# Performance work log

Hardware: AMD Instinct MI355X
Metric: run time of the kernel (lower is better)

Reference implementation:

```python
import jax, jax.numpy as jnp
import numpy as np

B, L, D = 16, 196, 512
M = 4096            # existing memory slots
DIS_MEM_LEN = 4096  # M+1 > DIS_MEM_LEN -> eviction always triggers (static shapes)


def setup_inputs() -> dict:
    key = jax.random.key(0)
    ks = jax.random.split(key, 10)
    x = jax.random.normal(ks[0], (B, L, D), jnp.float32)
    feat_mem = jax.random.normal(ks[1], (B, M, D), jnp.float32)
    # freq >= 6 so rm_mask = (freq > 5) is guaranteed nonempty (matches torch
    # branch `if rm_mask.sum() > 0`) and asserts freq != 0, min <= freq hold.
    freq_mem = 6 + jax.random.randint(ks[2], (B, M), 0, 50, jnp.int32)
    min_mem = jax.random.randint(ks[3], (B, M), 0, 6, jnp.int32)
    s = float(1.0 / np.sqrt(D))
    Wv = jax.random.uniform(ks[4], (D, D), jnp.float32, -s, s)
    bv = jax.random.uniform(ks[5], (D,), jnp.float32, -s, s)
    Wu = jax.random.uniform(ks[6], (D, D), jnp.float32, -s, s)
    bu = jax.random.uniform(ks[7], (D,), jnp.float32, -s, s)
    Ww = jax.random.uniform(ks[8], (D, 1), jnp.float32, -s, s)
    bw = jax.random.uniform(ks[9], (1,), jnp.float32, -s, s)
    return dict(x=x, feat_mem=feat_mem, freq_mem=freq_mem, min_mem=min_mem,
                Wv=Wv, bv=bv, Wu=Wu, bu=bu, Ww=Ww, bw=bw)


def reference(x, feat_mem, freq_mem, min_mem, Wv, bv, Wu, bu, Ww, bw):
    bs = x.shape[0]
    cls = x[:, :1, :]                                  # [B, 1, D]
    feat = jnp.concatenate([feat_mem, cls], axis=1)    # [B, M+1, D]
    zero = jnp.zeros((bs, 1), jnp.int32)
    freq = jnp.concatenate([freq_mem, zero], axis=1)   # [B, M+1]
    mn = jnp.concatenate([min_mem, zero], axis=1)      # [B, M+1]

    # gated attention score: sigmoid(Linear(tanh(Lv x) * sigmoid(Lu x)))
    attn_v = jnp.tanh(feat @ Wv + bv)
    attn_u = jax.nn.sigmoid(feat @ Wu + bu)
    attn_score = jax.nn.sigmoid((attn_v * attn_u) @ Ww + bw)  # [B, M+1, 1]

    # eval-mode cur_iter_mask = ones; feat is detached in z in the original
    z = jnp.sum(attn_score * jax.lax.stop_gradient(feat), axis=1)  # [B, D]

    # update_freq_mem: mask is all ones -> +1 everywhere
    freq = freq + 1
    # update_min_mem: argmin of attn_score along memory dim, scatter +1
    attn_idx = jnp.argmin(attn_score[..., 0], axis=1)  # [B]
    mn = mn.at[jnp.arange(bs), attn_idx].add(1)

    # eviction: M+1 > dis_mem_len, remove argmax(min/freq * (freq>5)) per batch
    rm_mask = freq > 5
    ratio = mn.astype(jnp.float32) / freq.astype(jnp.float32) * rm_mask
    rm_idx = jnp.argmax(ratio, axis=1)                 # [B]
    col = jnp.arange(freq.shape[1])[None, :]
    is_rm = col == rm_idx[:, None]                     # [B, M+1] one True per row
    # stable argsort puts kept indices first (in original order), removed one last
    order = jnp.argsort(is_rm, axis=1, stable=True)[:, : freq.shape[1] - 1]
    feat_out = jnp.take_along_axis(feat, order[..., None], axis=1)  # [B, M, D]
    freq_out = jnp.take_along_axis(freq, order, axis=1)             # [B, M]
    min_out = jnp.take_along_axis(mn, order, axis=1)                # [B, M]
    return z, feat_out, freq_out, min_out
```

## Files before the change

kernel.cpp:

```cpp
#include <hip/hip_runtime.h>
#include <cmath>

#define NB 16
#define MM 4096
#define MP1 4097
#define DD 512
#define LSEQ 196
#define NRB 65
#define MARGIN 0.05f
#define CANDMAX 128

typedef float f32x4 __attribute__((ext_vector_type(4)));
typedef short bf16x8 __attribute__((ext_vector_type(8)));
typedef unsigned short u16x8 __attribute__((ext_vector_type(8)));

static __device__ __forceinline__ unsigned short bf16_rne(float x) {
  union { float f; unsigned u; } c; c.f = x;
  unsigned u = c.u;
  u += 0x7fffu + ((u >> 16) & 1u);
  return (unsigned short)(u >> 16);
}
static __device__ __forceinline__ float bf16_to_f(unsigned short h) {
  union { unsigned u; float f; } c; c.u = ((unsigned)h) << 16;
  return c.f;
}
static __device__ __forceinline__ unsigned cvt_pk_bf16(float lo, float hi) {
  unsigned r;
  asm("v_cvt_pk_bf16_f32 %0, %1, %2" : "=v"(r) : "v"(lo), "v"(hi));
  return r;
}
static __device__ __forceinline__ float sig_prec(float v) { return 1.0f / (1.0f + expf(-v)); }
static __device__ __forceinline__ float sig_fast(float v) { return 1.0f / (1.0f + __expf(-v)); }
static __device__ __forceinline__ float tanh_fast(float v) { return fmaf(2.0f, sig_fast(2.0f * v), -1.0f); }

__global__ __launch_bounds__(256) void k_packW(const float* __restrict__ Wv,
                                               const float* __restrict__ Wu,
                                               unsigned short* __restrict__ Bc) {
  const int gid = blockIdx.x * 256 + threadIdx.x;
  const int l = gid & 63;
  const int ksg = (gid >> 6) & 15;
  const int ctg = (gid >> 10) & 31;
  const int mat = gid >> 15;
  const float* W = mat ? Wu : Wv;
  const int col = ctg * 16 + (l & 15);
  const int kb = ksg * 32 + (l >> 4) * 8;
  u16x8 hi;
#pragma unroll
  for (int i = 0; i < 8; ++i) hi[i] = bf16_rne(W[(size_t)(kb + i) * DD + col]);
  const int ctg2 = ctg * 2 + mat;
  *(u16x8*)(Bc + ((size_t)(ctg2 * 16 + ksg)) * 512 + l * 8) = hi;
}

__global__ __launch_bounds__(1024) void k_scores(
    const float* __restrict__ x, const float* __restrict__ feat_mem,
    const unsigned short* __restrict__ Bc,
    const float* __restrict__ bv, const float* __restrict__ bu,
    const float* __restrict__ Ww, const float* __restrict__ bw,
    float* __restrict__ logits, float* __restrict__ zacc) {
  const int rb = blockIdx.x, b = blockIdx.y;
  const int row0 = rb * 64;
  const int tid = threadIdx.x, wave = tid >> 6, l = tid & 63;

  __shared__ __align__(16) unsigned short A[4 * 8192];
  __shared__ float sred[16][64];
  __shared__ float sscore[64];

  {
    const int r = tid >> 4;
    const int j = tid & 15;
    const int grow = row0 + r;
    const float* srcrow = nullptr;
    if (grow < MM) srcrow = feat_mem + ((size_t)b * MM + grow) * DD;
    else if (grow == MM) srcrow = x + (size_t)b * LSEQ * DD;
    const int rt = r >> 4, lrow = r & 15;
#pragma unroll
    for (int it = 0; it < 8; ++it) {
      const int k0 = it * 64 + j * 4;
      const float4 v = srcrow ? *(const float4*)(srcrow + k0) : make_float4(0.f, 0.f, 0.f, 0.f);
      const int kc = k0 >> 7, kin = k0 & 127;
      const int ks = kin >> 5, lhi = (kin >> 3) & 3, ii = kin & 7;
      uint2 p;
      p.x = cvt_pk_bf16(v.x, v.y);
      p.y = cvt_pk_bf16(v.z, v.w);
      *(uint2*)(A + kc * 8192 + (ks * 4 + rt) * 512 + (lhi * 16 + lrow) * 8 + ii) = p;
    }
  }
  __syncthreads();

  f32x4 acc[4][4];
#pragma unroll
  for (int i = 0; i < 4; ++i)
#pragma unroll
    for (int j2 = 0; j2 < 4; ++j2) acc[i][j2] = (f32x4){0.f, 0.f, 0.f, 0.f};

  const unsigned short* Bwave = Bc + ((size_t)(wave * 4) * 16) * 512 + l * 8;
#pragma unroll 4
  for (int ksg = 0; ksg < 16; ++ksg) {
    const unsigned short* Ab = A + (ksg >> 2) * 8192 + ((ksg & 3) * 4) * 512 + l * 8;
    bf16x8 hiA[4];
#pragma unroll
    for (int rt = 0; rt < 4; ++rt) hiA[rt] = *(const bf16x8*)(Ab + rt * 512);
#pragma unroll
    for (int ct = 0; ct < 4; ++ct) {
      const bf16x8 bb = *(const bf16x8*)(Bwave + (size_t)(ct * 16 + ksg) * 512);
#pragma unroll
      for (int rt = 0; rt < 4; ++rt)
        acc[rt][ct] = __builtin_amdgcn_mfma_f32_16x16x32_bf16(hiA[rt], bb, acc[rt][ct], 0, 0, 0);
    }
  }

  float prow[4][4];
#pragma unroll
  for (int i = 0; i < 4; ++i)
#pragma unroll
    for (int j2 = 0; j2 < 4; ++j2) prow[i][j2] = 0.f;
#pragma unroll
  for (int gp = 0; gp < 2; ++gp) {
    const int col = (wave * 2 + gp) * 16 + (l & 15);
    const float bvc = bv[col], buc = bu[col], wwc = Ww[col];
#pragma unroll
    for (int rt = 0; rt < 4; ++rt)
#pragma unroll
      for (int rr = 0; rr < 4; ++rr) {
        const float vv = tanh_fast(acc[rt][2 * gp][rr] + bvc);
        const float uu = sig_fast(acc[rt][2 * gp + 1][rr] + buc);
        prow[rt][rr] = fmaf(vv * uu, wwc, prow[rt][rr]);
      }
  }
#pragma unroll
  for (int off = 1; off < 16; off <<= 1)
#pragma unroll
    for (int rt = 0; rt < 4; ++rt)
#pragma unroll
      for (int rr = 0; rr < 4; ++rr) prow[rt][rr] += __shfl_xor(prow[rt][rr], off, 64);

  if ((l & 15) == 0) {
#pragma unroll
    for (int rt = 0; rt < 4; ++rt)
#pragma unroll
      for (int rr = 0; rr < 4; ++rr) sred[wave][rt * 16 + (l >> 4) * 4 + rr] = prow[rt][rr];
  }
  __syncthreads();

  if (tid < 64) {
    float s = 0.f;
#pragma unroll
    for (int w = 0; w < 16; ++w) s += sred[w][tid];
    const int row = row0 + tid;
    if (row < MP1) logits[(size_t)b * MP1 + row] = s;
    sscore[tid] = sig_fast(s + bw[0]);
  }
  __syncthreads();

  {
    const int d = tid & 511;
    const int rh = tid >> 9;
    const int kc = d >> 7, kin = d & 127;
    const int ks = kin >> 5, lhi = (kin >> 3) & 3, ii = kin & 7;
    const unsigned short* Abase = A + kc * 8192 + ks * 4 * 512 + lhi * 16 * 8 + ii;
    float zp = 0.f;
#pragma unroll
    for (int rr2 = 0; rr2 < 32; ++rr2) {
      const int r2 = rh * 32 + rr2;
      const float a = bf16_to_f(Abase[(r2 >> 4) * 512 + (r2 & 15) * 8]);
      zp = fmaf(sscore[r2], a, zp);
    }
    atomicAdd(&zacc[(size_t)b * DD + d], zp);
  }
}

__global__ __launch_bounds__(256) void k_cand(const float* __restrict__ logits,
                                              int* __restrict__ cand,
                                              int* __restrict__ cnt) {
  const int b = blockIdx.x, tid = threadIdx.x;
  __shared__ float sv[256];
  __shared__ int scnt;
  float m = INFINITY;
  for (int i = tid; i < MP1; i += 256) m = fminf(m, logits[(size_t)b * MP1 + i]);
  sv[tid] = m;
  __syncthreads();
  for (int s = 128; s >= 1; s >>= 1) {
    if (tid < s) sv[tid] = fminf(sv[tid], sv[tid + s]);
    __syncthreads();
  }
  const float minv = sv[0];
  if (tid == 0) scnt = 0;
  __syncthreads();
  for (int i = tid; i < MP1; i += 256) {
    if (logits[(size_t)b * MP1 + i] <= minv + MARGIN) {
      const int p = atomicAdd(&scnt, 1);
      if (p < CANDMAX) cand[b * CANDMAX + p] = i;
    }
  }
  __syncthreads();
  if (tid == 0) cnt[b] = (scnt < CANDMAX) ? scnt : CANDMAX;
}

__global__ __launch_bounds__(256) void k_refine(
    const float* __restrict__ x, const float* __restrict__ feat_mem,
    const float* __restrict__ Wv, const float* __restrict__ bv,
    const float* __restrict__ Wu, const float* __restrict__ bu,
    const float* __restrict__ Ww,
    const int* __restrict__ cand, const int* __restrict__ cnt,
    float* __restrict__ candpart) {
  const int b = blockIdx.z, c = blockIdx.y, cb = blockIdx.x;
  if (c >= cnt[b]) return;
  const int row = cand[b * CANDMAX + c];
  const int tid = threadIdx.x;
  const int jl = tid & 63;
  const int ks = tid >> 6;
  const int col = cb * 64 + jl;
  __shared__ __align__(16) float sfeat[DD];
  __shared__ float sredv[4][64];
  __shared__ float sredu[4][64];
  const float* src = (row < MM) ? feat_mem + ((size_t)b * MM + row) * DD
                                : x + (size_t)b * LSEQ * DD;
  if (tid < 128) ((float4*)sfeat)[tid] = ((const float4*)src)[tid];
  __syncthreads();
  float v = 0.f, u = 0.f;
  const float* wvp = Wv + (size_t)(ks * 128) * DD + col;
  const float* wup = Wu + (size_t)(ks * 128) * DD + col;
#pragma unroll 8
  for (int k = 0; k < 128; ++k) {
    const float a = sfeat[ks * 128 + k];
    v = fmaf(a, wvp[(size_t)k * DD], v);
    u = fmaf(a, wup[(size_t)k * DD], u);
  }
  sredv[ks][jl] = v;
  sredu[ks][jl] = u;
  __syncthreads();
  if (tid < 64) {
    const float vv = (sredv[0][jl] + sredv[1][jl]) + (sredv[2][jl] + sredv[3][jl]);
    const float uu = (sredu[0][jl] + sredu[1][jl]) + (sredu[2][jl] + sredu[3][jl]);
    float g = tanhf(vv + bv[col]) * sig_prec(uu + bu[col]) * Ww[col];
#pragma unroll
    for (int off = 1; off < 64; off <<= 1) g += __shfl_xor(g, off, 64);
    if (jl == 0) candpart[((size_t)b * CANDMAX + c) * 8 + cb] = g;
  }
}

__global__ __launch_bounds__(256) void k_finalize2(
    const int* __restrict__ cand, const float* __restrict__ candpart,
    const int* __restrict__ cnt, const int* __restrict__ freq_mem,
    const int* __restrict__ min_mem, const float* __restrict__ zacc,
    float* __restrict__ out_z, float* __restrict__ out_freq,
    float* __restrict__ out_min, int* __restrict__ rm_attn) {
  const int b = blockIdx.x, tid = threadIdx.x;
  __shared__ float sv[256];
  __shared__ int si[256];
  __shared__ int sn[256], sd[256], sj[256];
  __shared__ int s_attn, s_rm;

  const int n = cnt[b];
  float v = INFINITY;
  int idx = MP1;
  if (tid < n) {
    const float* p = candpart + ((size_t)b * CANDMAX + tid) * 8;
    v = ((p[0] + p[1]) + (p[2] + p[3])) + ((p[4] + p[5]) + (p[6] + p[7]));
    idx = cand[b * CANDMAX + tid];
  }
  sv[tid] = v; si[tid] = idx;
  __syncthreads();
  for (int s = 128; s >= 1; s >>= 1) {
    if (tid < s) {
      const float v2 = sv[tid + s]; const int i2 = si[tid + s];
      if (v2 < sv[tid] || (v2 == sv[tid] && i2 < si[tid])) { sv[tid] = v2; si[tid] = i2; }
    }
    __syncthreads();
  }
  if (tid == 0) s_attn = si[0];
  __syncthreads();
  const int attn = s_attn;

  int bn = -1, bd = 1, bj = 0;
  for (int i = tid; i < MP1; i += 256) {
    int num, den;
    if (i < MM) {
      den = freq_mem[(size_t)b * MM + i] + 1;
      num = min_mem[(size_t)b * MM + i] + (i == attn ? 1 : 0);
      if (den <= 5) num = 0;
    } else { den = 1; num = 0; }
    if (num * bd > bn * den) { bn = num; bd = den; bj = i; }
  }
  sn[tid] = bn; sd[tid] = bd; sj[tid] = bj;
  __syncthreads();
  for (int s = 128; s >= 1; s >>= 1) {
    if (tid < s) {
      const int n2 = sn[tid + s], d2 = sd[tid + s], j2 = sj[tid + s];
      const int lft = n2 * sd[tid], rgt = sn[tid] * d2;
      if (lft > rgt || (lft == rgt && j2 < sj[tid])) { sn[tid] = n2; sd[tid] = d2; sj[tid] = j2; }
    }
    __syncthreads();
  }
  if (tid == 0) { s_rm = sj[0]; rm_attn[b * 2] = attn; rm_attn[b * 2 + 1] = sj[0]; }
  __syncthreads();
  const int rm = s_rm;

  for (int i = tid; i < MM; i += 256) {
    const int src = (i < rm) ? i : i + 1;
    int fv, mv;
    if (src < MM) {
      fv = freq_mem[(size_t)b * MM + src] + 1;
      mv = min_mem[(size_t)b * MM + src] + (src == attn ? 1 : 0);
    } else {
      fv = 1; mv = (attn == MM) ? 1 : 0;
    }
    out_freq[(size_t)b * MM + i] = (float)fv;
    out_min[(size_t)b * MM + i] = (float)mv;
  }
  for (int d = tid; d < DD; d += 256) out_z[(size_t)b * DD + d] = zacc[(size_t)b * DD + d];
}

__global__ __launch_bounds__(256) void k_gather(
    const float* __restrict__ feat_mem, const float* __restrict__ x,
    const int* __restrict__ rm_attn, float* __restrict__ out_feat) {
  const int b = blockIdx.y;
  const int rm = rm_attn[b * 2 + 1];
  const int row = blockIdx.x * 4 + (threadIdx.x >> 6);
  const int lane = threadIdx.x & 63;
  const int src = (row < rm) ? row : row + 1;
  const float* sp = (src < MM) ? (feat_mem + ((size_t)b * MM + src) * DD)
                               : (x + (size_t)b * LSEQ * DD);
  float* dp = out_feat + ((size_t)b * MM + row) * DD;
  const float4 v0 = reinterpret_cast<const float4*>(sp)[lane];
  const float4 v1 = reinterpret_cast<const float4*>(sp)[lane + 64];
  reinterpret_cast<float4*>(dp)[lane] = v0;
  reinterpret_cast<float4*>(dp)[lane + 64] = v1;
}

extern "C" void kernel_launch(void* const* d_in, const int* in_sizes, int n_in,
                              void* d_out, int out_size, void* d_ws, size_t ws_size,
                              hipStream_t stream) {
  const float* x        = (const float*)d_in[0];
  const float* feat_mem = (const float*)d_in[1];
  const int*   freq_mem = (const int*)d_in[2];
  const int*   min_mem  = (const int*)d_in[3];
  const float* Wv       = (const float*)d_in[4];
  const float* bv       = (const float*)d_in[5];
  const float* Wu       = (const float*)d_in[6];
  const float* bu       = (const float*)d_in[7];
  const float* Ww       = (const float*)d_in[8];
  const float* bw       = (const float*)d_in[9];

  float* ws       = (float*)d_ws;
  float* logits   = ws;
  float* zacc     = ws + NB * MP1;
  float* candpart = zacc + NB * DD;
  int*   cand     = (int*)(candpart + NB * CANDMAX * 8);
  int*   cnt      = cand + NB * CANDMAX;
  int*   rm_attn  = cnt + NB;
  unsigned short* Bc = (unsigned short*)(rm_attn + 32);

  float* out_z    = (float*)d_out;
  float* out_feat = out_z + NB * DD;
  float* out_freq = out_feat + (size_t)NB * MM * DD;
  float* out_min  = out_freq + (size_t)NB * MM;

  hipMemsetAsync(zacc, 0, NB * DD * sizeof(float), stream);
  hipMemsetAsync(cnt, 0, NB * sizeof(int), stream);

  k_packW<<<dim3(256), dim3(256), 0, stream>>>(Wv, Wu, Bc);
  k_scores<<<dim3(NRB, NB), dim3(1024), 0, stream>>>(x, feat_mem, Bc, bv, bu, Ww, bw,
                                                     logits, zacc);
  k_cand<<<dim3(NB), dim3(256), 0, stream>>>(logits, cand, cnt);
  k_refine<<<dim3(8, CANDMAX, NB), dim3(256), 0, stream>>>(x, feat_mem, Wv, bv, Wu, bu, Ww,
                                                           cand, cnt, candpart);
  k_finalize2<<<dim3(NB), dim3(256), 0, stream>>>(cand, candpart, cnt, freq_mem, min_mem, zacc,
                                                  out_z, out_freq, out_min, rm_attn);
  k_gather<<<dim3(MM / 4, NB), dim3(256), 0, stream>>>(feat_mem, x, rm_attn, out_feat);
}
```

Measured before the change: 224.1 us.

## Swizzle LDS A-tile layout, double-buffer B fragment loads, batch global loads

```diff
diff --git a/kernel.cpp b/kernel.cpp
--- a/kernel.cpp
+++ b/kernel.cpp
@@ -73,16 +73,22 @@
     if (grow < MM) srcrow = feat_mem + ((size_t)b * MM + grow) * DD;
     else if (grow == MM) srcrow = x + (size_t)b * LSEQ * DD;
     const int rt = r >> 4, lrow = r & 15;
+    float4 v[8];
+#pragma unroll
+    for (int it = 0; it < 8; ++it)
+      v[it] = srcrow ? *(const float4*)(srcrow + it * 64 + j * 4)
+                     : make_float4(0.f, 0.f, 0.f, 0.f);
 #pragma unroll
     for (int it = 0; it < 8; ++it) {
       const int k0 = it * 64 + j * 4;
-      const float4 v = srcrow ? *(const float4*)(srcrow + k0) : make_float4(0.f, 0.f, 0.f, 0.f);
       const int kc = k0 >> 7, kin = k0 & 127;
       const int ks = kin >> 5, lhi = (kin >> 3) & 3, ii = kin & 7;
       uint2 p;
-      p.x = cvt_pk_bf16(v.x, v.y);
-      p.y = cvt_pk_bf16(v.z, v.w);
-      *(uint2*)(A + kc * 8192 + (ks * 4 + rt) * 512 + (lhi * 16 + lrow) * 8 + ii) = p;
+      p.x = cvt_pk_bf16(v[it].x, v[it].y);
+      p.y = cvt_pk_bf16(v[it].z, v[it].w);
+      const int U = kc * 8192 + (ks * 4 + rt) * 512 + lhi * 128 +
+                    ((lrow * 8) ^ (lhi << 3) ^ ((ks & 1) << 5)) + ii;
+      *(uint2*)(A + U) = p;
     }
   }
   __syncthreads();
@@ -94,20 +100,41 @@
     for (int j2 = 0; j2 < 4; ++j2) acc[i][j2] = (f32x4){0.f, 0.f, 0.f, 0.f};
 
   const unsigned short* Bwave = Bc + ((size_t)(wave * 4) * 16) * 512 + l * 8;
-#pragma unroll 4
-  for (int ksg = 0; ksg < 16; ++ksg) {
-    const unsigned short* Ab = A + (ksg >> 2) * 8192 + ((ksg & 3) * 4) * 512 + l * 8;
-    bf16x8 hiA[4];
-#pragma unroll
-    for (int rt = 0; rt < 4; ++rt) hiA[rt] = *(const bf16x8*)(Ab + rt * 512);
-#pragma unroll
-    for (int ct = 0; ct < 4; ++ct) {
-      const bf16x8 bb = *(const bf16x8*)(Bwave + (size_t)(ct * 16 + ksg) * 512);
-#pragma unroll
-      for (int rt = 0; rt < 4; ++rt)
-        acc[rt][ct] = __builtin_amdgcn_mfma_f32_16x16x32_bf16(hiA[rt], bb, acc[rt][ct], 0, 0, 0);
-    }
-  }
+  const int lanebase = l * 8 ^ ((l >> 4) << 3);
+  bf16x8 bbA[4], bbB[4];
+
+#define BLOAD(dst, ksg)                                                     \
+  {                                                                         \
+    _Pragma("unroll")                                                       \
+    for (int ct = 0; ct < 4; ++ct)                                          \
+      dst[ct] = *(const bf16x8*)(Bwave + (size_t)(ct * 16 + (ksg)) * 512);  \
+  }
+#define KSTEP(CUR, NXT, ksg, last)                                                        \
+  {                                                                                       \
+    if (!(last)) BLOAD(NXT, (ksg) + 1);                                                   \
+    const unsigned short* Ab =                                                            \
+        A + ((ksg) >> 2) * 8192 + ((ksg) & 3) * 2048 + (lanebase ^ (((ksg) & 1) << 5));   \
+    const bf16x8 hiA0 = *(const bf16x8*)(Ab);                                             \
+    const bf16x8 hiA1 = *(const bf16x8*)(Ab + 512);                                       \
+    const bf16x8 hiA2 = *(const bf16x8*)(Ab + 1024);                                      \
+    const bf16x8 hiA3 = *(const bf16x8*)(Ab + 1536);                                      \
+    _Pragma("unroll")                                                                     \
+    for (int ct = 0; ct < 4; ++ct) {                                                      \
+      acc[0][ct] = __builtin_amdgcn_mfma_f32_16x16x32_bf16(hiA0, CUR[ct], acc[0][ct], 0, 0, 0); \
+      acc[1][ct] = __builtin_amdgcn_mfma_f32_16x16x32_bf16(hiA1, CUR[ct], acc[1][ct], 0, 0, 0); \
+      acc[2][ct] = __builtin_amdgcn_mfma_f32_16x16x32_bf16(hiA2, CUR[ct], acc[2][ct], 0, 0, 0); \
+      acc[3][ct] = __builtin_amdgcn_mfma_f32_16x16x32_bf16(hiA3, CUR[ct], acc[3][ct], 0, 0, 0); \
+    }                                                                                     \
+  }
+
+  BLOAD(bbA, 0);
+#pragma unroll
+  for (int kk = 0; kk < 8; ++kk) {
+    KSTEP(bbA, bbB, 2 * kk, false);
+    KSTEP(bbB, bbA, 2 * kk + 1, (kk == 7));
+  }
+#undef BLOAD
+#undef KSTEP
 
   float prow[4][4];
 #pragma unroll
@@ -157,13 +184,14 @@
     const int rh = tid >> 9;
     const int kc = d >> 7, kin = d & 127;
     const int ks = kin >> 5, lhi = (kin >> 3) & 3, ii = kin & 7;
-    const unsigned short* Abase = A + kc * 8192 + ks * 4 * 512 + lhi * 16 * 8 + ii;
+    const int ubase = kc * 8192 + ks * 2048 + lhi * 128 + ii;
+    const int swz = (lhi << 3) ^ ((ks & 1) << 5);
     float zp = 0.f;
 #pragma unroll
     for (int rr2 = 0; rr2 < 32; ++rr2) {
       const int r2 = rh * 32 + rr2;
-      const float a = bf16_to_f(Abase[(r2 >> 4) * 512 + (r2 & 15) * 8]);
-      zp = fmaf(sscore[r2], a, zp);
+      const int U = ubase + (r2 >> 4) * 512 + (((r2 & 15) * 8) ^ swz);
+      zp = fmaf(sscore[r2], bf16_to_f(A[U]), zp);
     }
     atomicAdd(&zacc[(size_t)b * DD + d], zp);
   }
```

After: 252.9 us. 1.13x slower.

## Retile score GEMM to 32-row blocks with swizzled LDS and B prefetch

Applied to the files above, without the earlier changes.

```diff
diff --git a/kernel.cpp b/kernel.cpp
--- a/kernel.cpp
+++ b/kernel.cpp
@@ -6,7 +6,8 @@
 #define MP1 4097
 #define DD 512
 #define LSEQ 196
-#define NRB 65
+#define RWS 32
+#define NRB 129
 #define MARGIN 0.05f
 #define CANDMAX 128
 
@@ -51,19 +52,19 @@
   *(u16x8*)(Bc + ((size_t)(ctg2 * 16 + ksg)) * 512 + l * 8) = hi;
 }
 
-__global__ __launch_bounds__(1024) void k_scores(
+__global__ __launch_bounds__(512, 4) void k_scores(
     const float* __restrict__ x, const float* __restrict__ feat_mem,
     const unsigned short* __restrict__ Bc,
     const float* __restrict__ bv, const float* __restrict__ bu,
     const float* __restrict__ Ww, const float* __restrict__ bw,
     float* __restrict__ logits, float* __restrict__ zacc) {
   const int rb = blockIdx.x, b = blockIdx.y;
-  const int row0 = rb * 64;
+  const int row0 = rb * RWS;
   const int tid = threadIdx.x, wave = tid >> 6, l = tid & 63;
 
-  __shared__ __align__(16) unsigned short A[4 * 8192];
-  __shared__ float sred[16][64];
-  __shared__ float sscore[64];
+  __shared__ __align__(16) unsigned short A[32 * 512];
+  __shared__ float sred[8][RWS];
+  __shared__ float sscore[RWS];
 
   {
     const int r = tid >> 4;
@@ -77,49 +78,66 @@
     for (int it = 0; it < 8; ++it) {
       const int k0 = it * 64 + j * 4;
       const float4 v = srcrow ? *(const float4*)(srcrow + k0) : make_float4(0.f, 0.f, 0.f, 0.f);
-      const int kc = k0 >> 7, kin = k0 & 127;
-      const int ks = kin >> 5, lhi = (kin >> 3) & 3, ii = kin & 7;
+      const int ksg = k0 >> 5, lhi = (k0 >> 3) & 3, ii = k0 & 7;
       uint2 p;
       p.x = cvt_pk_bf16(v.x, v.y);
       p.y = cvt_pk_bf16(v.z, v.w);
-      *(uint2*)(A + kc * 8192 + (ks * 4 + rt) * 512 + (lhi * 16 + lrow) * 8 + ii) = p;
-    }
-  }
-  __syncthreads();
-
-  f32x4 acc[4][4];
-#pragma unroll
-  for (int i = 0; i < 4; ++i)
-#pragma unroll
-    for (int j2 = 0; j2 < 4; ++j2) acc[i][j2] = (f32x4){0.f, 0.f, 0.f, 0.f};
-
-  const unsigned short* Bwave = Bc + ((size_t)(wave * 4) * 16) * 512 + l * 8;
-#pragma unroll 4
+      const int U = (ksg * 2 + rt) * 512 + lhi * 128 +
+                    ((lrow * 8) ^ (lhi << 3) ^ ((ksg & 1) << 5)) + ii;
+      *(uint2*)(A + U) = p;
+    }
+  }
+  __syncthreads();
+
+  f32x4 acc[2][8];
+#pragma unroll
+  for (int i = 0; i < 2; ++i)
+#pragma unroll
+    for (int j2 = 0; j2 < 8; ++j2) acc[i][j2] = (f32x4){0.f, 0.f, 0.f, 0.f};
+
+  const unsigned short* Bwave = Bc + ((size_t)(wave * 8) * 16) * 512 + l * 8;
+  const int lanebase = l * 8 ^ ((l >> 4) << 3);
+  bf16x8 bbA[4], bbB[4];
+
+#define HLOAD(dst, ksg, h)                                                            \
+  {                                                                                   \
+    _Pragma("unroll")                                                                 \
+    for (int ct = 0; ct < 4; ++ct)                                                    \
+      dst[ct] = *(const bf16x8*)(Bwave + (size_t)(((h) * 4 + ct) * 16 + (ksg)) * 512);\
+  }
+
+  HLOAD(bbA, 0, 0);
+#pragma unroll
   for (int ksg = 0; ksg < 16; ++ksg) {
-    const unsigned short* Ab = A + (ksg >> 2) * 8192 + ((ksg & 3) * 4) * 512 + l * 8;
-    bf16x8 hiA[4];
-#pragma unroll
-    for (int rt = 0; rt < 4; ++rt) hiA[rt] = *(const bf16x8*)(Ab + rt * 512);
+    HLOAD(bbB, ksg, 1);
+    const unsigned short* Ab = A + ksg * 1024 + (lanebase ^ ((ksg & 1) << 5));
+    const bf16x8 hiA0 = *(const bf16x8*)(Ab);
+    const bf16x8 hiA1 = *(const bf16x8*)(Ab + 512);
 #pragma unroll
     for (int ct = 0; ct < 4; ++ct) {
-      const bf16x8 bb = *(const bf16x8*)(Bwave + (size_t)(ct * 16 + ksg) * 512);
-#pragma unroll
-      for (int rt = 0; rt < 4; ++rt)
-        acc[rt][ct] = __builtin_amdgcn_mfma_f32_16x16x32_bf16(hiA[rt], bb, acc[rt][ct], 0, 0, 0);
-    }
-  }
-
-  float prow[4][4];
-#pragma unroll
-  for (int i = 0; i < 4; ++i)
+      acc[0][ct] = __builtin_amdgcn_mfma_f32_16x16x32_bf16(hiA0, bbA[ct], acc[0][ct], 0, 0, 0);
+      acc[1][ct] = __builtin_amdgcn_mfma_f32_16x16x32_bf16(hiA1, bbA[ct], acc[1][ct], 0, 0, 0);
+    }
+    if (ksg < 15) HLOAD(bbA, ksg + 1, 0);
+#pragma unroll
+    for (int ct = 0; ct < 4; ++ct) {
+      acc[0][4 + ct] = __builtin_amdgcn_mfma_f32_16x16x32_bf16(hiA0, bbB[ct], acc[0][4 + ct], 0, 0, 0);
+      acc[1][4 + ct] = __builtin_amdgcn_mfma_f32_16x16x32_bf16(hiA1, bbB[ct], acc[1][4 + ct], 0, 0, 0);
+    }
+  }
+#undef HLOAD
+
+  float prow[2][4];
+#pragma unroll
+  for (int i = 0; i < 2; ++i)
 #pragma unroll
     for (int j2 = 0; j2 < 4; ++j2) prow[i][j2] = 0.f;
 #pragma unroll
-  for (int gp = 0; gp < 2; ++gp) {
-    const int col = (wave * 2 + gp) * 16 + (l & 15);
+  for (int gp = 0; gp < 4; ++gp) {
+    const int col = (wave * 4 + gp) * 16 + (l & 15);
     const float bvc = bv[col], buc = bu[col], wwc = Ww[col];
 #pragma unroll
-    for (int rt = 0; rt < 4; ++rt)
+    for (int rt = 0; rt < 2; ++rt)
 #pragma unroll
       for (int rr = 0; rr < 4; ++rr) {
         const float vv = tanh_fast(acc[rt][2 * gp][rr] + bvc);
@@ -130,22 +148,22 @@
 #pragma unroll
   for (int off = 1; off < 16; off <<= 1)
 #pragma unroll
-    for (int rt = 0; rt < 4; ++rt)
+    for (int rt = 0; rt < 2; ++rt)
 #pragma unroll
       for (int rr = 0; rr < 4; ++rr) prow[rt][rr] += __shfl_xor(prow[rt][rr], off, 64);
 
   if ((l & 15) == 0) {
 #pragma unroll
-    for (int rt = 0; rt < 4; ++rt)
+    for (int rt = 0; rt < 2; ++rt)
 #pragma unroll
       for (int rr = 0; rr < 4; ++rr) sred[wave][rt * 16 + (l >> 4) * 4 + rr] = prow[rt][rr];
   }
   __syncthreads();
 
-  if (tid < 64) {
+  if (tid < RWS) {
     float s = 0.f;
 #pragma unroll
-    for (int w = 0; w < 16; ++w) s += sred[w][tid];
+    for (int w = 0; w < 8; ++w) s += sred[w][tid];
     const int row = row0 + tid;
     if (row < MP1) logits[(size_t)b * MP1 + row] = s;
     sscore[tid] = sig_fast(s + bw[0]);
@@ -153,17 +171,15 @@
   __syncthreads();
 
   {
-    const int d = tid & 511;
-    const int rh = tid >> 9;
-    const int kc = d >> 7, kin = d & 127;
-    const int ks = kin >> 5, lhi = (kin >> 3) & 3, ii = kin & 7;
-    const unsigned short* Abase = A + kc * 8192 + ks * 4 * 512 + lhi * 16 * 8 + ii;
+    const int d = tid;
+    const int ksg = d >> 5, lhi = (d >> 3) & 3, ii = d & 7;
+    const int ubase = ksg * 1024 + lhi * 128 + ii;
+    const int swz = (lhi << 3) ^ ((ksg & 1) << 5);
     float zp = 0.f;
 #pragma unroll
-    for (int rr2 = 0; rr2 < 32; ++rr2) {
-      const int r2 = rh * 32 + rr2;
-      const float a = bf16_to_f(Abase[(r2 >> 4) * 512 + (r2 & 15) * 8]);
-      zp = fmaf(sscore[r2], a, zp);
+    for (int r = 0; r < RWS; ++r) {
+      const int U = ubase + (r >> 4) * 512 + (((r & 15) * 8) ^ swz);
+      zp = fmaf(sscore[r], bf16_to_f(A[U]), zp);
     }
     atomicAdd(&zacc[(size_t)b * DD + d], zp);
   }
@@ -360,8 +376,8 @@
   hipMemsetAsync(cnt, 0, NB * sizeof(int), stream);
 
   k_packW<<<dim3(256), dim3(256), 0, stream>>>(Wv, Wu, Bc);
-  k_scores<<<dim3(NRB, NB), dim3(1024), 0, stream>>>(x, feat_mem, Bc, bv, bu, Ww, bw,
-                                                     logits, zacc);
+  k_scores<<<dim3(NRB, NB), dim3(512), 0, stream>>>(x, feat_mem, Bc, bv, bu, Ww, bw,
+                                                    logits, zacc);
   k_cand<<<dim3(NB), dim3(256), 0, stream>>>(logits, cand, cnt);
   k_refine<<<dim3(8, CANDMAX, NB), dim3(256), 0, stream>>>(x, feat_mem, Wv, bv, Wu, bu, Ww,
                                                            cand, cnt, candpart);
```

Result: slower. 269.6 us (+20.3%).
